# Kernel tuning notes

Hardware: AMD Instinct MI355X
Metric: run time of the kernel (lower is better)

## Reference

```python
import jax, jax.numpy as jnp
import numpy as np

MAX_SH_DEGREE = 3
NUM_BASES = (MAX_SH_DEGREE + 1) ** 2  # 16


def eval_sh_bases_fast(dirs):
    """SH bases up to degree 3 for unit directions [..., 3] -> [..., 16].
    Matches gsplat's _eval_sh_bases_fast constants/order."""
    x, y, z = dirs[..., 0], dirs[..., 1], dirs[..., 2]
    z2 = z * z
    fTmp0B = -1.092548430592079 * z
    fC1 = x * x - y * y
    fS1 = 2.0 * x * y
    fTmp0C = -2.285228997322329 * z2 + 0.4570457994644658
    fTmp1B = 1.445305721320277 * z
    fC2 = x * fC1 - y * fS1
    fS2 = x * fS1 + y * fC1
    ones = jnp.full_like(x, 0.2820947917738781)
    return jnp.stack([
        ones,
        -0.48860251190292 * y,
        0.48860251190292 * z,
        -0.48860251190292 * x,
        0.5462742152960395 * fS1,
        fTmp0B * y,
        0.9461746957575601 * z2 - 0.3153915652525201,
        fTmp0B * x,
        0.5462742152960395 * fC1,
        -0.5900435899266435 * fS2,
        fTmp1B * fS1,
        fTmp0C * y,
        z * (1.865881662950577 * z2 - 1.119528997770346),
        fTmp0C * x,
        fTmp1B * fC1,
        -0.5900435899266435 * fC2,
    ], axis=-1)


def setup_inputs() -> dict:
    key = jax.random.key(0)
    ks = jax.random.split(key, 10)
    C, N, F, E, W = 4, 250000, 32, 16, 128
    D_IN = E + F + NUM_BASES  # 64
    return {
        "features": jax.random.normal(ks[0], (N, F), jnp.float32),
        "dirs": jax.random.normal(ks[1], (C, N, 3), jnp.float32),
        "embed_table": jax.random.normal(ks[2], (1000, E), jnp.float32) * 0.1,
        "W0": jax.random.normal(ks[3], (D_IN, W), jnp.float32) / np.sqrt(D_IN),
        "b0": jax.random.normal(ks[4], (W,), jnp.float32) * 0.01,
        "W1": jax.random.normal(ks[5], (W, W), jnp.float32) / np.sqrt(W),
        "b1": jax.random.normal(ks[6], (W,), jnp.float32) * 0.01,
        "W2": jax.random.normal(ks[7], (W, 3), jnp.float32) / np.sqrt(W),
        "b2": jax.random.normal(ks[8], (3,), jnp.float32) * 0.01,
        "embed_ids": jax.random.randint(ks[9], (C,), 0, 1000, jnp.int64 if jax.config.jax_enable_x64 else jnp.int32),
        "sh_degree": 3,
    }


def reference(features, dirs, embed_table, W0, b0, W1, b1, W2, b2, embed_ids, sh_degree):
    C, N = dirs.shape[:2]
    E = embed_table.shape[1]
    F_dim = features.shape[1]
    # camera embeddings broadcast over splats
    emb = embed_table[embed_ids]                                   # [C, E]
    emb = jnp.broadcast_to(emb[:, None, :], (C, N, E))
    feats = jnp.broadcast_to(features[None, :, :], (C, N, F_dim))
    # F.normalize(dirs, dim=-1): divide by norm clamped at eps=1e-12
    norm = jnp.linalg.norm(dirs, axis=-1, keepdims=True)
    nd = dirs / jnp.maximum(norm, 1e-12)
    nb_use = (sh_degree + 1) ** 2  # static python int
    sh = eval_sh_bases_fast(nd)                                    # [C, N, 16]
    if nb_use < NUM_BASES:  # zero bases beyond requested degree
        mask = (jnp.arange(NUM_BASES) < nb_use).astype(sh.dtype)
        sh = sh * mask
    x = jnp.concatenate([emb, feats, sh], axis=-1)                 # [C, N, 64]
    h = jax.nn.relu(x @ W0 + b0)
    h = jax.nn.relu(h @ W1 + b1)
    return h @ W2 + b2                                             # [C, N, 3]
```

## Files before the change

### kernel.cpp

```cpp
#include <hip/hip_runtime.h>
#include <cstdint>
#include <cstddef>

typedef _Float16 half8 __attribute__((ext_vector_type(8)));
typedef __fp16 fp16x2 __attribute__((ext_vector_type(2)));
typedef float floatx16 __attribute__((ext_vector_type(16)));
typedef unsigned uint2v __attribute__((ext_vector_type(2)));


__global__ void vdc_prep_kernel(const float* __restrict__ W0,
                                const float* __restrict__ W1,
                                const float* __restrict__ W2,
                                const float* __restrict__ b0,
                                const float* __restrict__ b1,
                                const float* __restrict__ b2,
                                const float* __restrict__ emb_tab,
                                const int* __restrict__ embed_ids,
                                int C,
                                _Float16* __restrict__ ws) {
    int i = blockIdx.x * 256 + threadIdx.x;
    int w0end = C * 8192;
    int w1end = w0end + 18432;
    int w2end = w1end + 4608;
    float v = 0.0f;
    if (i < w0end) {
        int c = i >> 13, r = i & 8191;
        int ci = r >> 9, l = (r >> 3) & 63, ii = r & 7;
        int mt = ci >> 2, ks = ci & 3;
        int j  = mt * 32 + (l & 31);
        int kk = ks * 16 + (l >> 5) * 8 + ii;
        if (kk < 48) v = W0[(16 + kk) * 128 + j];
        else if (kk == 48) {
            int id = embed_ids[c];
            v = b0[j];
            #pragma unroll
            for (int e = 0; e < 16; ++e)
                v += emb_tab[(size_t)id * 16 + e] * W0[e * 128 + j];
        }
        ws[i] = (_Float16)v;
    } else if (i < w1end) {
        int r = i - w0end;
        int ci = r >> 9, l = (r >> 3) & 63, ii = r & 7;
        int mt = ci / 9, ks = ci - mt * 9;
        int j  = mt * 32 + (l & 31);
        int kk = ks * 16 + (l >> 5) * 8 + ii;
        if (kk < 128) v = W1[kk * 128 + j];
        else if (kk == 128) v = b1[j];
        ws[i] = (_Float16)v;
    } else if (i < w2end) {
        int r = i - w1end;
        int ks = r >> 9, l = (r >> 3) & 63, ii = r & 7;
        int o  = l & 31;
        int kk = ks * 16 + (l >> 5) * 8 + ii;
        if (o < 3) {
            if (kk < 128) v = W2[kk * 3 + o];
            else if (kk == 128) v = b2[o];
        }
        ws[i] = (_Float16)v;
    }
}

union U4 { unsigned u[4]; half8 h; };

__device__ __forceinline__ unsigned pkr(float a, float b) {
    union { fp16x2 h; unsigned u; } x;
    x.h = __builtin_amdgcn_cvt_pkrtz(a, b);
    return x.u;
}

__device__ __forceinline__ unsigned pkrelu(float a, float b) {
    union { fp16x2 h; unsigned u; } x;
    x.h = __builtin_amdgcn_cvt_pkrtz(a, b);
    fp16x2 z = {(__fp16)0.0f, (__fp16)0.0f};
    x.h = __builtin_elementwise_max(x.h, z);
    return x.u;
}

__device__ __forceinline__ floatx16 zero16() {
    floatx16 z;
    #pragma unroll
    for (int r = 0; r < 16; ++r) z[r] = 0.0f;
    return z;
}

__device__ __forceinline__ void transition(const floatx16& a, int hl,
                                           half8& lo, half8& hi) {
    unsigned p0 = pkrelu(a[0],  a[1]);
    unsigned p1 = pkrelu(a[2],  a[3]);
    unsigned p2 = pkrelu(a[4],  a[5]);
    unsigned p3 = pkrelu(a[6],  a[7]);
    unsigned p4 = pkrelu(a[8],  a[9]);
    unsigned p5 = pkrelu(a[10], a[11]);
    unsigned p6 = pkrelu(a[12], a[13]);
    unsigned p7 = pkrelu(a[14], a[15]);
    U4 L, H;
#if __has_builtin(__builtin_amdgcn_permlane32_swap)
    uint2v s02 = __builtin_amdgcn_permlane32_swap(p0, p2, false, false);
    uint2v s13 = __builtin_amdgcn_permlane32_swap(p1, p3, false, false);
    uint2v s46 = __builtin_amdgcn_permlane32_swap(p4, p6, false, false);
    uint2v s57 = __builtin_amdgcn_permlane32_swap(p5, p7, false, false);
    L.u[0] = s02[0]; L.u[1] = s13[0]; L.u[2] = s02[1]; L.u[3] = s13[1];
    H.u[0] = s46[0]; H.u[1] = s57[0]; H.u[2] = s46[1]; H.u[3] = s57[1];
    (void)hl;
#else
    unsigned r0 = __shfl_xor(hl ? p0 : p2, 32);
    unsigned r1 = __shfl_xor(hl ? p1 : p3, 32);
    unsigned r2 = __shfl_xor(hl ? p4 : p6, 32);
    unsigned r3 = __shfl_xor(hl ? p5 : p7, 32);
    L.u[0] = hl ? r0 : p0;
    L.u[1] = hl ? r1 : p1;
    L.u[2] = hl ? p2 : r0;
    L.u[3] = hl ? p3 : r1;
    H.u[0] = hl ? r2 : p4;
    H.u[1] = hl ? r3 : p5;
    H.u[2] = hl ? p6 : r2;
    H.u[3] = hl ? p7 : r3;
#endif
    lo = L.h; hi = H.h;
}

__device__ __forceinline__ void build_bfrags(
    const float* __restrict__ feats, const float* __restrict__ dirs,
    size_t cN, int n, int hl, int nbu,
    half8& o0, half8& o1, half8& o2)
{
    const float* fp = feats + (size_t)n * 32 + hl * 8;
    float4 f0 = *(const float4*)(fp);
    float4 f1 = *(const float4*)(fp + 4);
    float4 f2 = *(const float4*)(fp + 16);
    float4 f3 = *(const float4*)(fp + 20);
    U4 u0, u1;
    u0.u[0] = pkr(f0.x, f0.y); u0.u[1] = pkr(f0.z, f0.w);
    u0.u[2] = pkr(f1.x, f1.y); u0.u[3] = pkr(f1.z, f1.w);
    u1.u[0] = pkr(f2.x, f2.y); u1.u[1] = pkr(f2.z, f2.w);
    u1.u[2] = pkr(f3.x, f3.y); u1.u[3] = pkr(f3.z, f3.w);
    o0 = u0.h; o1 = u1.h;

    const float* dp = dirs + (cN + n) * 3;
    float dx = dp[0], dy = dp[1], dz = dp[2];
    float nrm = sqrtf(dx * dx + dy * dy + dz * dz);
    float inv = 1.0f / fmaxf(nrm, 1e-12f);
    float x = dx * inv, y = dy * inv, z = dz * inv;

    float z2     = z * z;
    float fTmp0B = -1.092548430592079f * z;
    float fC1    = x * x - y * y;
    float fS1    = 2.0f * x * y;
    float fTmp0C = -2.285228997322329f * z2 + 0.4570457994644658f;
    float fTmp1B = 1.445305721320277f * z;
    float fC2    = x * fC1 - y * fS1;
    float fS2    = x * fS1 + y * fC1;

    float sh[16];
    sh[0]  = 0.2820947917738781f;
    sh[1]  = -0.48860251190292f * y;
    sh[2]  = 0.48860251190292f * z;
    sh[3]  = -0.48860251190292f * x;
    sh[4]  = 0.5462742152960395f * fS1;
    sh[5]  = fTmp0B * y;
    sh[6]  = 0.9461746957575601f * z2 - 0.3153915652525201f;
    sh[7]  = fTmp0B * x;
    sh[8]  = 0.5462742152960395f * fC1;
    sh[9]  = -0.5900435899266435f * fS2;
    sh[10] = fTmp1B * fS1;
    sh[11] = fTmp0C * y;
    sh[12] = z * (1.865881662950577f * z2 - 1.119528997770346f);
    sh[13] = fTmp0C * x;
    sh[14] = fTmp1B * fC1;
    sh[15] = -0.5900435899266435f * fC2;
    #pragma unroll
    for (int i = 0; i < 16; ++i) if (i >= nbu) sh[i] = 0.0f;

    float s0 = hl ? sh[8]  : sh[0];
    float s1 = hl ? sh[9]  : sh[1];
    float s2 = hl ? sh[10] : sh[2];
    float s3 = hl ? sh[11] : sh[3];
    float s4 = hl ? sh[12] : sh[4];
    float s5 = hl ? sh[13] : sh[5];
    float s6 = hl ? sh[14] : sh[6];
    float s7 = hl ? sh[15] : sh[7];
    U4 u2;
    u2.u[0] = pkr(s0, s1); u2.u[1] = pkr(s2, s3);
    u2.u[2] = pkr(s4, s5); u2.u[3] = pkr(s6, s7);
    o2 = u2.h;
}

#define MFMA(a, b, c) __builtin_amdgcn_mfma_f32_32x32x16_f16((a), (b), (c), 0, 0, 0)
#define LDF(off) (*(const half8*)(fr + (off)))
#define GW2(ch) (*(const half8*)(w2p + (ch) * 512 + lane * 8))

#define L0_MT(MT, HA0, HA1, HB0, HB1)                                    \
    do {                                                                 \
        floatx16 ca = zero16();                                          \
        floatx16 cb = zero16();                                          \
        half8 t0 = LDF(((MT) * 4 + 0) * 1024);                           \
        ca = MFMA(t0, ax0, ca); cb = MFMA(t0, bx0, cb);                  \
        half8 t1 = LDF(((MT) * 4 + 1) * 1024);                           \
        ca = MFMA(t1, ax1, ca); cb = MFMA(t1, bx1, cb);                  \
        half8 t2 = LDF(((MT) * 4 + 2) * 1024);                           \
        ca = MFMA(t2, ax2, ca); cb = MFMA(t2, bx2, cb);                  \
        half8 t3 = LDF(((MT) * 4 + 3) * 1024);                           \
        ca = MFMA(t3, bbias, ca); cb = MFMA(t3, bbias, cb);              \
        transition(ca, hl, HA0, HA1);                                    \
        transition(cb, hl, HB0, HB1);                                    \
    } while (0)

#define L1_KS(MT, KS, HA, HB)                                            \
    do {                                                                 \
        half8 q = LDF(16384 + ((MT) * 9 + (KS)) * 1024);                 \
        ca = MFMA(q, HA, ca); cb = MFMA(q, HB, cb);                      \
    } while (0)

#define L1_MT(MT)                                                        \
    do {                                                                 \
        floatx16 ca = zero16();                                          \
        floatx16 cb = zero16();                                          \
        L1_KS(MT, 0, ha0, hb0);                                          \
        L1_KS(MT, 1, ha1, hb1);                                          \
        L1_KS(MT, 2, ha2, hb2);                                          \
        L1_KS(MT, 3, ha3, hb3);                                          \
        L1_KS(MT, 4, ha4, hb4);                                          \
        L1_KS(MT, 5, ha5, hb5);                                          \
        L1_KS(MT, 6, ha6, hb6);                                          \
        L1_KS(MT, 7, ha7, hb7);                                          \
        L1_KS(MT, 8, bbias, bbias);                                      \
        half8 w2a = GW2(2 * (MT) + 0);                                   \
        half8 w2b = GW2(2 * (MT) + 1);                                   \
        half8 g0, g1;                                                    \
        transition(ca, hl, g0, g1);                                      \
        acc3a = MFMA(w2a, g0, acc3a); acc3a = MFMA(w2b, g1, acc3a);      \
        transition(cb, hl, g0, g1);                                      \
        acc3b = MFMA(w2a, g0, acc3b); acc3b = MFMA(w2b, g1, acc3b);      \
    } while (0)

__global__ __launch_bounds__(256, 3) void vdc_mlp_kernel(
    const float* __restrict__ feats,
    const float* __restrict__ dirs,
    const int* __restrict__ sh_deg_p,
    const _Float16* __restrict__ ws,
    float* __restrict__ out,
    int N, int C)
{
    __shared__ uint4 arena[3328];
    char* lds = (char*)arena;

    const int tid   = threadIdx.x;
    const int c     = blockIdx.y;
    const int w     = tid >> 6;
    const int lane  = tid & 63;
    const int ln    = lane & 31;
    const int hl    = lane >> 5;
    const int base  = blockIdx.x * 256 + w * 64;

    const _Float16* w2p = ws + (size_t)C * 8192 + 18432;

    {
        const uint4* srcA = (const uint4*)(ws + (size_t)c * 8192);
        const uint4* srcB = (const uint4*)(ws + (size_t)C * 8192);
        #pragma unroll
        for (int it = 0; it < 13; ++it) {
            int idx = it * 256 + tid;
            arena[idx] = (idx < 1024) ? srcA[idx] : srcB[idx - 1024];
        }
    }

    half8 bbias;
    {
        U4 ub;
        ub.u[0] = hl ? 0u : 0x00003C00u;
        ub.u[1] = 0u; ub.u[2] = 0u; ub.u[3] = 0u;
        bbias = ub.h;
    }
    int deg = sh_deg_p[0];
    int nbu = (deg + 1) * (deg + 1);
    int na = base + ln;      if (na >= N) na = N - 1;
    int nb = base + 32 + ln; if (nb >= N) nb = N - 1;
    half8 ax0, ax1, ax2, bx0, bx1, bx2;
    build_bfrags(feats, dirs, (size_t)c * N, na, hl, nbu, ax0, ax1, ax2);
    build_bfrags(feats, dirs, (size_t)c * N, nb, hl, nbu, bx0, bx1, bx2);

    __syncthreads();

    const char* fr = lds + lane * 16;

    half8 ha0, ha1, ha2, ha3, ha4, ha5, ha6, ha7;
    half8 hb0, hb1, hb2, hb3, hb4, hb5, hb6, hb7;
    L0_MT(0, ha0, ha1, hb0, hb1);
    L0_MT(1, ha2, ha3, hb2, hb3);
    L0_MT(2, ha4, ha5, hb4, hb5);
    L0_MT(3, ha6, ha7, hb6, hb7);

    floatx16 acc3a = zero16();
    floatx16 acc3b = zero16();
    L1_MT(0);
    L1_MT(1);
    L1_MT(2);
    L1_MT(3);
    {
        half8 ab = GW2(8);
        acc3a = MFMA(ab, bbias, acc3a);
        acc3b = MFMA(ab, bbias, acc3b);
    }

    if (hl == 0) {
        int nn = base + ln;
        if (nn < N) {
            float* op = out + ((size_t)c * N + nn) * 3;
            op[0] = acc3a[0];
            op[1] = acc3a[1];
            op[2] = acc3a[2];
        }
        nn = base + 32 + ln;
        if (nn < N) {
            float* op = out + ((size_t)c * N + nn) * 3;
            op[0] = acc3b[0];
            op[1] = acc3b[1];
            op[2] = acc3b[2];
        }
    }
}

extern "C" void kernel_launch(void* const* d_in, const int* in_sizes, int n_in,
                              void* d_out, int out_size, void* d_ws, size_t ws_size,
                              hipStream_t stream) {
    const float* feats   = (const float*)d_in[0];
    const float* dirs    = (const float*)d_in[1];
    const float* emb_tab = (const float*)d_in[2];
    const float* W0      = (const float*)d_in[3];
    const float* b0      = (const float*)d_in[4];
    const float* W1      = (const float*)d_in[5];
    const float* b1      = (const float*)d_in[6];
    const float* W2      = (const float*)d_in[7];
    const float* b2      = (const float*)d_in[8];
    const int*   eids    = (const int*)d_in[9];
    const int*   shd     = (const int*)d_in[10];
    float* outp          = (float*)d_out;

    int N = in_sizes[0] / 32;
    int C = in_sizes[9];

    _Float16* wsh = (_Float16*)d_ws;

    int ws_elems = C * 8192 + 23040;
    vdc_prep_kernel<<<(ws_elems + 255) / 256, 256, 0, stream>>>(
        W0, W1, W2, b0, b1, b2, emb_tab, eids, C, wsh);

    dim3 grid((N + 255) / 256, C);
    vdc_mlp_kernel<<<grid, 256, 0, stream>>>(
        feats, dirs, shd, wsh, outp, N, C);
}
```

Before: 147.3 us.

## Halve per-wave point tile, load W0 from global, split L1 accumulators

Each wave now handles 32 points instead of 64, so the second set of B fragments and accumulators goes away, and occupancy is raised to 4 blocks per CU. Layer-0 weights are read straight from global/L2 instead of LDS, which shrinks the shared arena, and layer-1 uses two interleaved accumulators to break the serial MFMA dependency chain. The aim is more waves in flight to hide latency. The trade-off is that each LDS and global weight fragment is reused across half as many points, and the grid has twice as many blocks, each repeating the LDS fill.

```diff
diff --git a/kernel.cpp b/kernel.cpp
--- a/kernel.cpp
+++ b/kernel.cpp
@@ -187,53 +187,55 @@
 
 #define MFMA(a, b, c) __builtin_amdgcn_mfma_f32_32x32x16_f16((a), (b), (c), 0, 0, 0)
 #define LDF(off) (*(const half8*)(fr + (off)))
+#define GW0(ch) (*(const half8*)(w0p + (ch) * 512 + lane * 8))
 #define GW2(ch) (*(const half8*)(w2p + (ch) * 512 + lane * 8))
 
-#define L0_MT(MT, HA0, HA1, HB0, HB1)                                    \
+#define L0_MT(MT, H0, H1)                                                \
     do {                                                                 \
         floatx16 ca = zero16();                                          \
-        floatx16 cb = zero16();                                          \
-        half8 t0 = LDF(((MT) * 4 + 0) * 1024);                           \
-        ca = MFMA(t0, ax0, ca); cb = MFMA(t0, bx0, cb);                  \
-        half8 t1 = LDF(((MT) * 4 + 1) * 1024);                           \
-        ca = MFMA(t1, ax1, ca); cb = MFMA(t1, bx1, cb);                  \
-        half8 t2 = LDF(((MT) * 4 + 2) * 1024);                           \
-        ca = MFMA(t2, ax2, ca); cb = MFMA(t2, bx2, cb);                  \
-        half8 t3 = LDF(((MT) * 4 + 3) * 1024);                           \
-        ca = MFMA(t3, bbias, ca); cb = MFMA(t3, bbias, cb);              \
-        transition(ca, hl, HA0, HA1);                                    \
-        transition(cb, hl, HB0, HB1);                                    \
-    } while (0)
-
-#define L1_KS(MT, KS, HA, HB)                                            \
-    do {                                                                 \
-        half8 q = LDF(16384 + ((MT) * 9 + (KS)) * 1024);                 \
-        ca = MFMA(q, HA, ca); cb = MFMA(q, HB, cb);                      \
+        half8 t0 = GW0((MT) * 4 + 0);                                    \
+        half8 t1 = GW0((MT) * 4 + 1);                                    \
+        half8 t2 = GW0((MT) * 4 + 2);                                    \
+        half8 t3 = GW0((MT) * 4 + 3);                                    \
+        ca = MFMA(t0, ax0, ca);                                          \
+        ca = MFMA(t1, ax1, ca);                                          \
+        ca = MFMA(t2, ax2, ca);                                          \
+        ca = MFMA(t3, bbias, ca);                                        \
+        transition(ca, hl, H0, H1);                                      \
     } while (0)
 
 #define L1_MT(MT)                                                        \
     do {                                                                 \
-        floatx16 ca = zero16();                                          \
-        floatx16 cb = zero16();                                          \
-        L1_KS(MT, 0, ha0, hb0);                                          \
-        L1_KS(MT, 1, ha1, hb1);                                          \
-        L1_KS(MT, 2, ha2, hb2);                                          \
-        L1_KS(MT, 3, ha3, hb3);                                          \
-        L1_KS(MT, 4, ha4, hb4);                                          \
-        L1_KS(MT, 5, ha5, hb5);                                          \
-        L1_KS(MT, 6, ha6, hb6);                                          \
-        L1_KS(MT, 7, ha7, hb7);                                          \
-        L1_KS(MT, 8, bbias, bbias);                                      \
+        floatx16 c0 = zero16();                                          \
+        floatx16 c1 = zero16();                                          \
+        half8 q0 = LDF(((MT) * 9 + 0) * 1024);                           \
+        c0 = MFMA(q0, ha0, c0);                                          \
+        half8 q1 = LDF(((MT) * 9 + 1) * 1024);                           \
+        c1 = MFMA(q1, ha1, c1);                                          \
+        half8 q2 = LDF(((MT) * 9 + 2) * 1024);                           \
+        c0 = MFMA(q2, ha2, c0);                                          \
+        half8 q3 = LDF(((MT) * 9 + 3) * 1024);                           \
+        c1 = MFMA(q3, ha3, c1);                                          \
+        half8 q4 = LDF(((MT) * 9 + 4) * 1024);                           \
+        c0 = MFMA(q4, ha4, c0);                                          \
+        half8 q5 = LDF(((MT) * 9 + 5) * 1024);                           \
+        c1 = MFMA(q5, ha5, c1);                                          \
+        half8 q6 = LDF(((MT) * 9 + 6) * 1024);                           \
+        c0 = MFMA(q6, ha6, c0);                                          \
+        half8 q7 = LDF(((MT) * 9 + 7) * 1024);                           \
+        c1 = MFMA(q7, ha7, c1);                                          \
+        half8 q8 = LDF(((MT) * 9 + 8) * 1024);                           \
+        c0 = MFMA(q8, bbias, c0);                                        \
+        floatx16 cs = c0 + c1;                                           \
+        half8 g0, g1;                                                    \
+        transition(cs, hl, g0, g1);                                      \
         half8 w2a = GW2(2 * (MT) + 0);                                   \
         half8 w2b = GW2(2 * (MT) + 1);                                   \
-        half8 g0, g1;                                                    \
-        transition(ca, hl, g0, g1);                                      \
-        acc3a = MFMA(w2a, g0, acc3a); acc3a = MFMA(w2b, g1, acc3a);      \
-        transition(cb, hl, g0, g1);                                      \
-        acc3b = MFMA(w2a, g0, acc3b); acc3b = MFMA(w2b, g1, acc3b);      \
+        acc3 = MFMA(w2a, g0, acc3);                                      \
+        acc3 = MFMA(w2b, g1, acc3);                                      \
     } while (0)
 
-__global__ __launch_bounds__(256, 3) void vdc_mlp_kernel(
+__global__ __launch_bounds__(256, 4) void vdc_mlp_kernel(
     const float* __restrict__ feats,
     const float* __restrict__ dirs,
     const int* __restrict__ sh_deg_p,
@@ -241,7 +243,7 @@
     float* __restrict__ out,
     int N, int C)
 {
-    __shared__ uint4 arena[3328];
+    __shared__ uint4 arena[2304];
     char* lds = (char*)arena;
 
     const int tid   = threadIdx.x;
@@ -250,17 +252,17 @@
     const int lane  = tid & 63;
     const int ln    = lane & 31;
     const int hl    = lane >> 5;
-    const int base  = blockIdx.x * 256 + w * 64;
-
+    const int base  = blockIdx.x * 128 + w * 32;
+
+    const _Float16* w0p = ws + (size_t)c * 8192;
     const _Float16* w2p = ws + (size_t)C * 8192 + 18432;
 
     {
-        const uint4* srcA = (const uint4*)(ws + (size_t)c * 8192);
-        const uint4* srcB = (const uint4*)(ws + (size_t)C * 8192);
+        const uint4* src = (const uint4*)(ws + (size_t)C * 8192);
         #pragma unroll
-        for (int it = 0; it < 13; ++it) {
+        for (int it = 0; it < 9; ++it) {
             int idx = it * 256 + tid;
-            arena[idx] = (idx < 1024) ? srcA[idx] : srcB[idx - 1024];
+            arena[idx] = src[idx];
         }
     }
 
@@ -273,49 +275,37 @@
     }
     int deg = sh_deg_p[0];
     int nbu = (deg + 1) * (deg + 1);
-    int na = base + ln;      if (na >= N) na = N - 1;
-    int nb = base + 32 + ln; if (nb >= N) nb = N - 1;
-    half8 ax0, ax1, ax2, bx0, bx1, bx2;
+    int na = base + ln; if (na >= N) na = N - 1;
+    half8 ax0, ax1, ax2;
     build_bfrags(feats, dirs, (size_t)c * N, na, hl, nbu, ax0, ax1, ax2);
-    build_bfrags(feats, dirs, (size_t)c * N, nb, hl, nbu, bx0, bx1, bx2);
 
     __syncthreads();
 
     const char* fr = lds + lane * 16;
 
     half8 ha0, ha1, ha2, ha3, ha4, ha5, ha6, ha7;
-    half8 hb0, hb1, hb2, hb3, hb4, hb5, hb6, hb7;
-    L0_MT(0, ha0, ha1, hb0, hb1);
-    L0_MT(1, ha2, ha3, hb2, hb3);
-    L0_MT(2, ha4, ha5, hb4, hb5);
-    L0_MT(3, ha6, ha7, hb6, hb7);
-
-    floatx16 acc3a = zero16();
-    floatx16 acc3b = zero16();
+    L0_MT(0, ha0, ha1);
+    L0_MT(1, ha2, ha3);
+    L0_MT(2, ha4, ha5);
+    L0_MT(3, ha6, ha7);
+
+    floatx16 acc3 = zero16();
     L1_MT(0);
     L1_MT(1);
     L1_MT(2);
     L1_MT(3);
     {
         half8 ab = GW2(8);
-        acc3a = MFMA(ab, bbias, acc3a);
-        acc3b = MFMA(ab, bbias, acc3b);
+        acc3 = MFMA(ab, bbias, acc3);
     }
 
     if (hl == 0) {
         int nn = base + ln;
         if (nn < N) {
             float* op = out + ((size_t)c * N + nn) * 3;
-            op[0] = acc3a[0];
-            op[1] = acc3a[1];
-            op[2] = acc3a[2];
-        }
-        nn = base + 32 + ln;
-        if (nn < N) {
-            float* op = out + ((size_t)c * N + nn) * 3;
-            op[0] = acc3b[0];
-            op[1] = acc3b[1];
-            op[2] = acc3b[2];
+            op[0] = acc3[0];
+            op[1] = acc3[1];
+            op[2] = acc3[2];
         }
     }
 }
@@ -345,7 +335,7 @@
     vdc_prep_kernel<<<(ws_elems + 255) / 256, 256, 0, stream>>>(
         W0, W1, W2, b0, b1, b2, emb_tab, eids, C, wsh);
 
-    dim3 grid((N + 255) / 256, C);
+    dim3 grid((N + 127) / 128, C);
     vdc_mlp_kernel<<<grid, 256, 0, stream>>>(
         feats, dirs, shd, wsh, outp, N, C);
 }
```

Result: slower. 156.4 us (+6.2%).
